# Kernel optimization log

Hardware: AMD Instinct MI355X
Metric: run time of the kernel (lower is better)

## Reference

```python
import jax, jax.numpy as jnp
import numpy as np

B, N, C, H, L, M, V, NC = 8, 2048, 512, 8, 8, 128, 32000, 2
HD = C // H          # head dim = 64
HID = 4 * C          # MLP hidden = 2048
SCALE = HD ** -0.5
LN_EPS = 1e-5
FEAT_EPS = 1e-6


def _orth_matrix(d, m, rng):
    # gaussian_orthogonal_random_matrix: stack QR blocks of d x d
    blocks = []
    n_full, m_rem = divmod(m, d)
    for _ in range(n_full):
        Q, _ = np.linalg.qr(rng.standard_normal((d, d)))
        blocks.append(Q)
    if m_rem > 0:
        Q, _ = np.linalg.qr(rng.standard_normal((d, d)))
        blocks.append(Q[:, :m_rem])
    return np.concatenate(blocks, axis=1)


def setup_inputs() -> dict:
    key = jax.random.key(0)
    ks = jax.random.split(key, 32)
    rng = np.random.default_rng(0)

    def w(i, shape, s=0.02):
        return jax.random.normal(ks[i], shape, jnp.float32) * s

    proj = jnp.asarray(
        np.stack([np.stack([_orth_matrix(HD, M, rng) for _ in range(H)]) for _ in range(L)]),
        jnp.float32)  # [L, H, HD, M]

    inp = {
        "input_ids": jax.random.randint(ks[0], (B, N), 0, V),
        "attention_mask": jnp.ones((B, N), jnp.int32),
        "tok_emb": w(1, (V, C)),
        "cls": w(2, (1, 1, C)),
        "pos": w(3, (N + 1, C)),
        "ln1_g": jnp.ones((L, C), jnp.float32),
        "ln1_b": jnp.zeros((L, C), jnp.float32),
        "qW": w(4, (L, C, C)), "qb": jnp.zeros((L, C), jnp.float32),
        "kW": w(5, (L, C, C)), "kb": jnp.zeros((L, C), jnp.float32),
        "vW": w(6, (L, C, C)), "vb": jnp.zeros((L, C), jnp.float32),
        "oW": w(7, (L, C, C)), "ob": jnp.zeros((L, C), jnp.float32),
        "proj": proj,
        "ln2_g": jnp.ones((L, C), jnp.float32),
        "ln2_b": jnp.zeros((L, C), jnp.float32),
        "fc1W": w(8, (L, C, HID)), "fc1b": jnp.zeros((L, HID), jnp.float32),
        "fc2W": w(9, (L, HID, C)), "fc2b": jnp.zeros((L, C), jnp.float32),
        "lnf_g": jnp.ones((C,), jnp.float32),
        "lnf_b": jnp.zeros((C,), jnp.float32),
        "headW": w(10, (C, NC)),
        "headb": jnp.zeros((NC,), jnp.float32),
    }
    return inp


def _ln(x, g, b):
    mu = jnp.mean(x, axis=-1, keepdims=True)
    var = jnp.mean((x - mu) ** 2, axis=-1, keepdims=True)
    return (x - mu) * jax.lax.rsqrt(var + LN_EPS) * g + b


def _softmax_feature(x, p):
    # x: [B,Nt,H,HD], p: [H,HD,M]
    xw = jnp.einsum('bnhd,hdm->bnhm', x, p)
    x_sq = 0.5 * jnp.sum(x * x, axis=-1, keepdims=True)
    mx = jnp.max(xw, axis=-1, keepdims=True)
    return jnp.exp(xw - mx) * jnp.exp(mx - x_sq) + FEAT_EPS


def reference(input_ids, attention_mask, tok_emb, cls, pos, ln1_g, ln1_b,
              qW, qb, kW, kb, vW, vb, oW, ob, proj, ln2_g, ln2_b,
              fc1W, fc1b, fc2W, fc2b, lnf_g, lnf_b, headW, headb):
    x = tok_emb[input_ids]                                   # [B,N,C]
    x = jnp.concatenate([jnp.broadcast_to(cls, (B, 1, C)), x], axis=1)  # [B,Nt,C]
    x = x + pos[None]
    mask = jnp.concatenate(
        [jnp.ones((B, 1), x.dtype), attention_mask.astype(x.dtype)], axis=1)  # [B,Nt]
    mfeat = mask[:, :, None, None]

    Nt = N + 1
    for i in range(L):
        # Performer attention (FAVOR+)
        y = _ln(x, ln1_g[i], ln1_b[i])
        q = (y @ qW[i] + qb[i]).reshape(B, Nt, H, HD) * SCALE
        k = (y @ kW[i] + kb[i]).reshape(B, Nt, H, HD) * mfeat
        v = (y @ vW[i] + vb[i]).reshape(B, Nt, H, HD) * mfeat
        qf = _softmax_feature(q, proj[i])                    # [B,Nt,H,M]
        kf = _softmax_feature(k, proj[i])
        kv = jnp.einsum('bnhm,bnhd->bhmd', kf, v)            # [B,H,M,HD]
        ksum = jnp.sum(kf, axis=1)                           # [B,H,M]
        denom = jnp.maximum(jnp.einsum('bnhm,bhm->bhn', qf, ksum), 1e-6)[..., None]
        ctx = jnp.einsum('bnhm,bhmd->bhnd', qf, kv) / denom  # [B,H,Nt,HD]
        out = ctx.transpose(0, 2, 1, 3).reshape(B, Nt, C)
        x = x + (out @ oW[i] + ob[i])
        # MLP (exact GELU, as nn.GELU default)
        y = _ln(x, ln2_g[i], ln2_b[i])
        h = jax.nn.gelu(y @ fc1W[i] + fc1b[i], approximate=False)
        x = x + (h @ fc2W[i] + fc2b[i])

    x = _ln(x, lnf_g, lnf_b)
    return x[:, 0] @ headW + headb                           # [B,NC]
```

## Files before the change

kernel.cpp:

```cpp
#include <hip/hip_runtime.h>
#include <cmath>
#include <cstdint>
#include <cstddef>

#define B_ 8
#define N_ 2048
#define NT 2049
#define NP 2080
#define C_ 512
#define H_ 8
#define HD_ 64
#define L_ 8
#define M_ 128
#define HID_ 2048
#define NC_ 2
#define BNT (B_*NT)
#define RP (B_*NP)
#define SCALE_ 0.125f
#define LN_EPS_ 1e-5f
#define FEAT_EPS_ 1e-6f

#define MODE_GELU  2
#define MODE_RESID 3

typedef unsigned short u16;
typedef unsigned short u16x8 __attribute__((ext_vector_type(8)));
typedef short frag __attribute__((ext_vector_type(8)));
typedef float f32x4 __attribute__((ext_vector_type(4)));

constexpr size_t F_X    = 0;
constexpr size_t F_KVP  = F_X   + (size_t)RP*512;
constexpr size_t F_KSP  = F_KVP + (size_t)4*64*8192;
constexpr size_t F_KV   = F_KSP + (size_t)4*64*128;
constexpr size_t F_KS   = F_KV  + (size_t)64*M_*HD_;
constexpr size_t F_QKVB = F_KS  + (size_t)64*M_;
constexpr size_t F_END  = F_QKVB + 1536;
constexpr size_t S_BASE = 2 * F_END;
constexpr size_t S_Y    = S_BASE;
constexpr size_t S_V    = S_Y  + (size_t)RP*512;
constexpr size_t S_KF   = S_V  + (size_t)RP*512;
constexpr size_t S_QF   = S_KF + (size_t)RP*1024;
constexpr size_t S_WQKV = S_QF + (size_t)RP*1024;
constexpr size_t S_WO   = S_WQKV + (size_t)1536*512;
constexpr size_t S_WF1  = S_WO   + (size_t)512*512;
constexpr size_t S_WF2  = S_WF1  + (size_t)2048*512;
constexpr size_t S_PT   = S_WF2  + (size_t)512*2048;
constexpr size_t S_END  = S_PT   + (size_t)8*128*64;
constexpr size_t WS_BYTES = S_END * 2;

__device__ __forceinline__ float wave_reduce(float v) {
#pragma unroll
  for (int off = 32; off > 0; off >>= 1) v += __shfl_down(v, off, 64);
  return v;
}
__device__ __forceinline__ float b2f(u16 u) {
  union { float f; uint32_t i; } v; v.i = ((uint32_t)u) << 16; return v.f;
}
__device__ __forceinline__ u16 f2b(float f) {
  union { float f; uint32_t i; } v; v.f = f;
  uint32_t r = v.i + 0x7FFF + ((v.i >> 16) & 1);
  return (u16)(r >> 16);
}
__device__ __forceinline__ void gstage(const u16* g, u16* lds_base, int lane) {
#if __has_builtin(__builtin_amdgcn_global_load_lds)
  __builtin_amdgcn_global_load_lds((const __attribute__((address_space(1))) void*)g,
      (__attribute__((address_space(3))) void*)lds_base, 16, 0, 0);
#else
  *(u16x8*)(lds_base + lane * 8) = *(const u16x8*)g;
#endif
}
__device__ __forceinline__ void xcd_swz(int& bx, int& by) {
  int gx = gridDim.x;
  int nwg = gx * gridDim.y;
  int hw = blockIdx.x + blockIdx.y * gx;
  if (nwg & 7) { bx = blockIdx.x; by = blockIdx.y; return; }
  int cpx = nwg >> 3;
  int swz = (hw & 7) * cpx + (hw >> 3);
  bx = swz % gx; by = swz / gx;
}

__global__ __launch_bounds__(256) void embed_k(const int* __restrict__ ids,
    const float* __restrict__ tok, const float* __restrict__ cls,
    const float* __restrict__ pos, float* __restrict__ X) {
  int row = blockIdx.x;
  int b = row / NT, n = row - b * NT;
  int t = threadIdx.x;
  const float* src = (n == 0) ? cls : tok + (size_t)ids[b * N_ + n - 1] * C_;
  size_t rp = (size_t)b * NP + n;
  X[rp * C_ + t]       = src[t]       + pos[(size_t)n * C_ + t];
  X[rp * C_ + t + 256] = src[t + 256] + pos[(size_t)n * C_ + t + 256];
}

__global__ __launch_bounds__(256) void wconv_k(
    const float* __restrict__ qW, const float* __restrict__ kW,
    const float* __restrict__ vW, const float* __restrict__ oW,
    const float* __restrict__ f1W, const float* __restrict__ f2W,
    const float* __restrict__ projL,
    const float* __restrict__ qb, const float* __restrict__ kb,
    const float* __restrict__ vb,
    u16* __restrict__ Wqkv, u16* __restrict__ Wo,
    u16* __restrict__ Wf1, u16* __restrict__ Wf2,
    u16* __restrict__ PT, float* __restrict__ QKVB) {
  __shared__ float tile[32][33];
  int bid = blockIdx.x, t = threadIdx.x;
  if (bid >= 3104) {
    int i = (bid - 3104) * 256 + t;
    QKVB[i] = (i < 512) ? qb[i] : (i < 1024) ? kb[i - 512] : vb[i - 1024];
    return;
  }
  if (bid >= 3072) {
    int base = (bid - 3072) * 2048 + t * 8;
#pragma unroll
    for (int j = 0; j < 8; ++j) {
      int idx = base + j;
      int h = idx >> 13, rem = idx & 8191, m = rem >> 6, d = rem & 63;
      PT[idx] = f2b(projL[(size_t)h * 8192 + d * 128 + m]);
    }
    return;
  }
  int ti = t >> 5, tj = t & 31;
  const float* src; u16* dst; int k0, n0, ldn, ldk, scol;
  if (bid < 768) {
    int tk = bid & 15, tn = bid >> 4;
    k0 = tk * 32; n0 = tn * 32;
    int sel = n0 >> 9; scol = n0 & 511;
    src = (sel == 0) ? qW : (sel == 1) ? kW : vW;
    ldn = 512; dst = Wqkv; ldk = 512;
  } else if (bid < 1024) {
    int b2 = bid - 768;
    int tk = b2 & 15, tn = b2 >> 4;
    k0 = tk * 32; n0 = tn * 32; scol = n0;
    src = oW; ldn = 512; dst = Wo; ldk = 512;
  } else if (bid < 2048) {
    int b2 = bid - 1024;
    int tk = b2 & 15, tn = b2 >> 4;
    k0 = tk * 32; n0 = tn * 32; scol = n0;
    src = f1W; ldn = 2048; dst = Wf1; ldk = 512;
  } else {
    int b2 = bid - 2048;
    int tk = b2 & 63, tn = b2 >> 6;
    k0 = tk * 32; n0 = tn * 32; scol = n0;
    src = f2W; ldn = 512; dst = Wf2; ldk = 2048;
  }
  const float* sp = src + (size_t)k0 * ldn + scol;
  u16* dp = dst + (size_t)n0 * ldk + k0;
#pragma unroll
  for (int p = 0; p < 4; ++p)
    tile[ti + p * 8][tj] = sp[(size_t)(ti + p * 8) * ldn + tj];
  __syncthreads();
#pragma unroll
  for (int p = 0; p < 4; ++p)
    dp[(size_t)(ti + p * 8) * ldk + tj] = f2b(tile[tj][ti + p * 8]);
}

__global__ __launch_bounds__(256) void ln_bf_k(const float* __restrict__ X,
    const float* __restrict__ g, const float* __restrict__ b,
    u16* __restrict__ Y) {
  int w = threadIdx.x >> 6, lane = threadIdx.x & 63;
  int row = blockIdx.x * 4 + w;
  const float* xr = X + (size_t)row * C_;
  float v[8];
  *(float4*)&v[0] = *(const float4*)(xr + lane * 8);
  *(float4*)&v[4] = *(const float4*)(xr + lane * 8 + 4);
  float s = 0.f;
#pragma unroll
  for (int j = 0; j < 8; ++j) s += v[j];
  s = wave_reduce(s);
  float mu = __shfl(s, 0, 64) * (1.0f / C_);
  float sq = 0.f;
#pragma unroll
  for (int j = 0; j < 8; ++j) { float d = v[j] - mu; sq = fmaf(d, d, sq); }
  sq = wave_reduce(sq);
  float rs = rsqrtf(__shfl(sq, 0, 64) * (1.0f / C_) + LN_EPS_);
  float gv[8], bv[8];
  *(float4*)&gv[0] = *(const float4*)(g + lane * 8);
  *(float4*)&gv[4] = *(const float4*)(g + lane * 8 + 4);
  *(float4*)&bv[0] = *(const float4*)(b + lane * 8);
  *(float4*)&bv[4] = *(const float4*)(b + lane * 8 + 4);
  u16x8 o;
#pragma unroll
  for (int j = 0; j < 8; ++j) o[j] = f2b((v[j] - mu) * rs * gv[j] + bv[j]);
  *(u16x8*)(Y + (size_t)row * C_ + lane * 8) = o;
}

__global__ __launch_bounds__(256) void gemm_bf_k(
    const u16* __restrict__ A, int lda,
    const u16* __restrict__ Wt,
    const float* __restrict__ bias,
    float* __restrict__ outF, u16* __restrict__ outB,
    int ldc, int Kdim, int mode) {
  __shared__ __align__(16) u16 As[2][128 * 64];
  __shared__ __align__(16) u16 Bs[2][128 * 64];
  const int t = threadIdx.x, w = t >> 6, l = t & 63;
  int bx, by; xcd_swz(bx, by);
  const int row0 = by * 128, col0 = bx * 128;
  const int wm = w & 1, wn = w >> 1;
  const int lm = l & 15, lkb = l >> 4;
  const int lr = l >> 3, lc = l & 7;
  const int kch = (lc ^ lr) * 8;
  const u16* Ag = A  + (size_t)(row0 + lr) * lda  + kch;
  const u16* Bg = Wt + (size_t)(col0 + lr) * Kdim + kch;
  const int sx = lm & 7;
  f32x4 acc[4][4] = {};
  const int nk = Kdim >> 6;
#pragma unroll
  for (int j = 0; j < 4; ++j) {
    int c8 = w * 4 + j;
    gstage(Ag + (size_t)c8 * 8 * lda , &As[0][c8 * 512], l);
    gstage(Bg + (size_t)c8 * 8 * Kdim, &Bs[0][c8 * 512], l);
  }
  for (int kt = 0; kt < nk; ++kt) {
    const int cur = kt & 1;
    if (kt + 1 < nk) {
      const int k0 = (kt + 1) << 6;
#pragma unroll
      for (int j = 0; j < 4; ++j) {
        int c8 = w * 4 + j;
        gstage(Ag + (size_t)c8 * 8 * lda  + k0, &As[cur ^ 1][c8 * 512], l);
        gstage(Bg + (size_t)c8 * 8 * Kdim + k0, &Bs[cur ^ 1][c8 * 512], l);
      }
      asm volatile("s_waitcnt vmcnt(8)" ::: "memory");
    } else {
      asm volatile("s_waitcnt vmcnt(0)" ::: "memory");
    }
    __builtin_amdgcn_s_barrier();
    __builtin_amdgcn_sched_barrier(0);
#pragma unroll
    for (int ks = 0; ks < 2; ++ks) {
      frag af[4], bf4[4];
#pragma unroll
      for (int i = 0; i < 4; ++i)
        af[i] = *(const frag*)&As[cur][(wm * 64 + i * 16 + lm) * 64 + (((ks * 4 + lkb) ^ sx) * 8)];
#pragma unroll
      for (int j = 0; j < 4; ++j)
        bf4[j] = *(const frag*)&Bs[cur][(wn * 64 + j * 16 + lm) * 64 + (((ks * 4 + lkb) ^ sx) * 8)];
#pragma unroll
      for (int i = 0; i < 4; ++i)
#pragma unroll
        for (int j = 0; j < 4; ++j)
          acc[i][j] = __builtin_amdgcn_mfma_f32_16x16x32_bf16(af[i], bf4[j], acc[i][j], 0, 0, 0);
    }
    __builtin_amdgcn_sched_barrier(0);
    __builtin_amdgcn_s_barrier();
  }
#pragma unroll
  for (int i = 0; i < 4; ++i) {
#pragma unroll
    for (int r = 0; r < 4; ++r) {
      int grow = row0 + wm * 64 + i * 16 + lkb * 4 + r;
      if (mode == MODE_RESID) {
        float* orow = outF + (size_t)grow * ldc + col0;
#pragma unroll
        for (int j = 0; j < 4; ++j) {
          int gc = wn * 64 + j * 16 + lm;
          orow[gc] += acc[i][j][r] + bias[col0 + gc];
        }
      } else {
        u16* orow = outB + (size_t)grow * ldc + col0;
#pragma unroll
        for (int j = 0; j < 4; ++j) {
          int gc = wn * 64 + j * 16 + lm;
          float v = acc[i][j][r] + bias[col0 + gc];
          float u = v * (1.5957691216f + 0.0713548162f * v * v);
          v = v / (1.f + __expf(-u));
          orow[gc] = f2b(v);
        }
      }
    }
  }
}

__global__ __launch_bounds__(256) void gemm_bf64_k(
    const u16* __restrict__ A, int lda,
    const u16* __restrict__ Wt,
    const float* __restrict__ bias,
    float* __restrict__ outF, u16* __restrict__ outB,
    int ldc, int Kdim, int mode) {
  __shared__ __align__(16) u16 As[2][64 * 64];
  __shared__ __align__(16) u16 Bs[2][128 * 64];
  const int t = threadIdx.x, w = t >> 6, l = t & 63;
  int bx, by; xcd_swz(bx, by);
  const int row0 = by * 64, col0 = bx * 128;
  const int wm = w & 1, wn = w >> 1;
  const int lm = l & 15, lkb = l >> 4;
  const int lr = l >> 3, lc = l & 7;
  const int kch = (lc ^ lr) * 8;
  const u16* Ag = A  + (size_t)(row0 + lr) * lda  + kch;
  const u16* Bg = Wt + (size_t)(col0 + lr) * Kdim + kch;
  const int sx = lm & 7;
  f32x4 acc[2][4] = {};
  const int nk = Kdim >> 6;
#pragma unroll
  for (int q = 0; q < 2; ++q) {
    int c8 = w * 2 + q;
    gstage(Ag + (size_t)c8 * 8 * lda, &As[0][c8 * 512], l);
  }
#pragma unroll
  for (int q = 0; q < 4; ++q) {
    int c8 = w * 4 + q;
    gstage(Bg + (size_t)c8 * 8 * Kdim, &Bs[0][c8 * 512], l);
  }
  for (int kt = 0; kt < nk; ++kt) {
    const int cur = kt & 1;
    if (kt + 1 < nk) {
      const int k0 = (kt + 1) << 6;
#pragma unroll
      for (int q = 0; q < 2; ++q) {
        int c8 = w * 2 + q;
        gstage(Ag + (size_t)c8 * 8 * lda + k0, &As[cur ^ 1][c8 * 512], l);
      }
#pragma unroll
      for (int q = 0; q < 4; ++q) {
        int c8 = w * 4 + q;
        gstage(Bg + (size_t)c8 * 8 * Kdim + k0, &Bs[cur ^ 1][c8 * 512], l);
      }
      asm volatile("s_waitcnt vmcnt(6)" ::: "memory");
    } else {
      asm volatile("s_waitcnt vmcnt(0)" ::: "memory");
    }
    __builtin_amdgcn_s_barrier();
    __builtin_amdgcn_sched_barrier(0);
#pragma unroll
    for (int ks = 0; ks < 2; ++ks) {
      frag af[2], bf4[4];
#pragma unroll
      for (int i = 0; i < 2; ++i)
        af[i] = *(const frag*)&As[cur][(wm * 32 + i * 16 + lm) * 64 + (((ks * 4 + lkb) ^ sx) * 8)];
#pragma unroll
      for (int j = 0; j < 4; ++j)
        bf4[j] = *(const frag*)&Bs[cur][(wn * 64 + j * 16 + lm) * 64 + (((ks * 4 + lkb) ^ sx) * 8)];
#pragma unroll
      for (int i = 0; i < 2; ++i)
#pragma unroll
        for (int j = 0; j < 4; ++j)
          acc[i][j] = __builtin_amdgcn_mfma_f32_16x16x32_bf16(af[i], bf4[j], acc[i][j], 0, 0, 0);
    }
    __builtin_amdgcn_sched_barrier(0);
    __builtin_amdgcn_s_barrier();
  }
#pragma unroll
  for (int i = 0; i < 2; ++i) {
#pragma unroll
    for (int r = 0; r < 4; ++r) {
      int grow = row0 + wm * 32 + i * 16 + lkb * 4 + r;
      if (mode == MODE_RESID) {
        float* orow = outF + (size_t)grow * ldc + col0;
#pragma unroll
        for (int j = 0; j < 4; ++j) {
          int gc = wn * 64 + j * 16 + lm;
          orow[gc] += acc[i][j][r] + bias[col0 + gc];
        }
      } else {
        u16* orow = outB + (size_t)grow * ldc + col0;
#pragma unroll
        for (int j = 0; j < 4; ++j) {
          int gc = wn * 64 + j * 16 + lm;
          float v = acc[i][j][r] + bias[col0 + gc];
          float u = v * (1.5957691216f + 0.0713548162f * v * v);
          v = v / (1.f + __expf(-u));
          orow[gc] = f2b(v);
        }
      }
    }
  }
}

__global__ __launch_bounds__(256) void gemmqkv_k(
    const u16* __restrict__ A,
    const u16* __restrict__ Wt,
    const float* __restrict__ bias,
    u16* __restrict__ Vout,
    u16* __restrict__ QF, u16* __restrict__ KF,
    const u16* __restrict__ PT,
    const int* __restrict__ attn) {
  __shared__ __align__(16) u16 As[128 * 64];
  __shared__ __align__(16) u16 Bs[128 * 64];
  __shared__ __align__(16) u16 ptb[128 * 64];
  __shared__ float sxe[128][2];
  const int t = threadIdx.x, w = t >> 6, l = t & 63;
  int bx, by; xcd_swz(bx, by);
  const int cx = bx;
  const int row0 = by * 128, col0 = cx * 128;
  const int wm = w & 1, wn = w >> 1;
  const int lm = l & 15, lkb = l >> 4;
  const int lr = l >> 3, lc = l & 7;
  const int kch = (lc ^ lr) * 8;
  const u16* Ag = A  + (size_t)(row0 + lr) * 512 + kch;
  const u16* Bg = Wt + (size_t)(col0 + lr) * 512 + kch;
  const int sx = lm & 7;
  f32x4 acc[4][4] = {};
  for (int k0 = 0; k0 < 512; k0 += 64) {
    __syncthreads();
#pragma unroll
    for (int j = 0; j < 4; ++j) {
      int c8 = w * 4 + j;
      gstage(Ag + (size_t)c8 * 8 * 512 + k0, &As[c8 * 512], l);
      gstage(Bg + (size_t)c8 * 8 * 512 + k0, &Bs[c8 * 512], l);
    }
    __syncthreads();
#pragma unroll
    for (int ks = 0; ks < 2; ++ks) {
      frag af[4], bf4[4];
#pragma unroll
      for (int i = 0; i < 4; ++i)
        af[i] = *(const frag*)&As[(wm * 64 + i * 16 + lm) * 64 + (((ks * 4 + lkb) ^ sx) * 8)];
#pragma unroll
      for (int j = 0; j < 4; ++j)
        bf4[j] = *(const frag*)&Bs[(wn * 64 + j * 16 + lm) * 64 + (((ks * 4 + lkb) ^ sx) * 8)];
#pragma unroll
      for (int i = 0; i < 4; ++i)
#pragma unroll
        for (int j = 0; j < 4; ++j)
          acc[i][j] = __builtin_amdgcn_mfma_f32_16x16x32_bf16(af[i], bf4[j], acc[i][j], 0, 0, 0);
    }
  }
  if (cx >= 8) {
    int c0v = col0 - 1024;
#pragma unroll
    for (int i = 0; i < 4; ++i) {
#pragma unroll
      for (int r = 0; r < 4; ++r) {
        int grow = row0 + wm * 64 + i * 16 + lkb * 4 + r;
        int bb = grow / NP, nn = grow - bb * NP;
        float mrow = (nn == 0) ? 1.f : ((nn < NT) ? (float)attn[bb * N_ + nn - 1] : 0.f);
        u16* orow = Vout + (size_t)grow * 512 + c0v;
#pragma unroll
        for (int j = 0; j < 4; ++j) {
          int gc = wn * 64 + j * 16 + lm;
          orow[gc] = f2b((acc[i][j][r] + bias[col0 + gc]) * mrow);
        }
      }
    }
    return;
  }
  const bool isq = (cx < 4);
  const int hbase = (isq ? cx : cx - 4) * 2;
  __syncthreads();
  {
    u16* qt = wn ? Bs : As;
#pragma unroll
    for (int i = 0; i < 4; ++i) {
#pragma unroll
      for (int r = 0; r < 4; ++r) {
        int rl = wm * 64 + i * 16 + lkb * 4 + r;
        float mrow;
        if (isq) mrow = SCALE_;
        else {
          int grow = row0 + rl;
          int bb = grow / NP, nn = grow - bb * NP;
          mrow = (nn == 0) ? 1.f : ((nn < NT) ? (float)attn[bb * N_ + nn - 1] : 0.f);
        }
#pragma unroll
        for (int j = 0; j < 4; ++j) {
          int gcc = j * 16 + lm;
          float v = (acc[i][j][r] + bias[col0 + wn * 64 + gcc]) * mrow;
          qt[rl * 64 + (((gcc >> 3) ^ (rl & 7)) * 8) + (gcc & 7)] = f2b(v);
        }
      }
    }
  }
  {
    const u16* Pg = PT + (size_t)hbase * 8192 + (size_t)lr * 64 + kch;
#pragma unroll
    for (int q = 0; q < 4; ++q) {
      int c8 = w * 4 + q;
      gstage(Pg + (size_t)c8 * 8 * 64, &ptb[c8 * 512], l);
    }
  }
  __syncthreads();
  {
    int rowi = t >> 1, hf = t & 1;
    const u16* qq = hf ? Bs : As;
    float s = 0.f;
#pragma unroll
    for (int c = 0; c < 8; ++c) {
      const u16* p = &qq[rowi * 64 + ((c ^ (rowi & 7)) * 8)];
#pragma unroll
      for (int e = 0; e < 8; ++e) { float a = b2f(p[e]); s = fmaf(a, a, s); }
    }
    sxe[rowi][hf] = 0.5f * s;
  }
  __syncthreads();
  u16* OF = isq ? QF : KF;
#pragma unroll
  for (int hp = 0; hp < 2; ++hp) {
    if (hp == 1) {
      __syncthreads();
      const u16* Pg = PT + (size_t)(hbase + 1) * 8192 + (size_t)lr * 64 + kch;
#pragma unroll
      for (int q = 0; q < 4; ++q) {
        int c8 = w * 4 + q;
        gstage(Pg + (size_t)c8 * 8 * 64, &ptb[c8 * 512], l);
      }
      __syncthreads();
    }
    const u16* qt = hp ? Bs : As;
    f32x4 a2[2][8] = {};
#pragma unroll
    for (int ks = 0; ks < 2; ++ks) {
      frag af2[2], bf2[8];
#pragma unroll
      for (int i = 0; i < 2; ++i)
        af2[i] = *(const frag*)&qt[(w * 32 + i * 16 + lm) * 64 + (((ks * 4 + lkb) ^ sx) * 8)];
#pragma unroll
      for (int j = 0; j < 8; ++j)
        bf2[j] = *(const frag*)&ptb[(j * 16 + lm) * 64 + (((ks * 4 + lkb) ^ sx) * 8)];
#pragma unroll
      for (int i = 0; i < 2; ++i)
#pragma unroll
        for (int j = 0; j < 8; ++j)
          a2[i][j] = __builtin_amdgcn_mfma_f32_16x16x32_bf16(af2[i], bf2[j], a2[i][j], 0, 0, 0);
    }
    int hg = hbase + hp;
#pragma unroll
    for (int i = 0; i < 2; ++i) {
#pragma unroll
      for (int r = 0; r < 4; ++r) {
        int R = w * 32 + i * 16 + lkb * 4 + r;
        int grow = row0 + R;
        int bb = grow / NP, nn = grow - bb * NP;
        bool valid = nn < NT;
        float xs = sxe[R][hp];
        u16* orow = OF + (size_t)grow * 1024 + (size_t)hg * 128;
#pragma unroll
        for (int j = 0; j < 8; ++j) {
          int m = j * 16 + lm;
          float v = valid ? (__expf(a2[i][j][r] - xs) + FEAT_EPS_) : 0.f;
          orow[m] = f2b(v);
        }
      }
    }
  }
}

__global__ __launch_bounds__(256) void kvpart_k(const u16* __restrict__ KF,
    const u16* __restrict__ Vb, float* __restrict__ KVP,
    float* __restrict__ KSP) {
  int ci = blockIdx.x, bh = blockIdx.y;
  int b = bh >> 3, h = bh & 7;
  size_t rb0 = (size_t)b * NP + ci * 520;
  __shared__ __align__(16) float kfs[8 * 132];
  __shared__ __align__(16) float vsm[8 * 68];
  int t = threadIdx.x;
  const int d0 = (t & 7) * 8, m0 = (t >> 3) * 4;
  const bool hk = t < 128;
  const bool hv = (t >= 128) && (t < 192);
  const int ktok = t >> 4, kmj = (t & 15) * 8;
  const int vtok = (t - 128) >> 3, vdj = (t & 7) * 8;
  float acc[4][8] = {};
  float ks[4] = {};
  u16x8 rk, rv;
  if (hk) rk = *(const u16x8*)&KF[(rb0 + ktok) * 1024 + h * 128 + kmj];
  if (hv) rv = *(const u16x8*)&Vb[(rb0 + vtok) * 512 + h * 64 + vdj];
  for (int tile = 0; tile < 65; ++tile) {
    if (hk) {
#pragma unroll
      for (int e = 0; e < 8; ++e) kfs[ktok * 132 + kmj + e] = b2f(rk[e]);
    }
    if (hv) {
#pragma unroll
      for (int e = 0; e < 8; ++e) vsm[vtok * 68 + vdj + e] = b2f(rv[e]);
    }
    __syncthreads();
    if (tile + 1 < 65) {
      size_t rb = rb0 + (size_t)(tile + 1) * 8;
      if (hk) rk = *(const u16x8*)&KF[(rb + ktok) * 1024 + h * 128 + kmj];
      if (hv) rv = *(const u16x8*)&Vb[(rb + vtok) * 512 + h * 64 + vdj];
    }
#pragma unroll
    for (int tok = 0; tok < 8; ++tok) {
      float kq[4], va[8];
      *(float4*)&kq[0] = *(const float4*)&kfs[tok * 132 + m0];
      *(float4*)&va[0] = *(const float4*)&vsm[tok * 68 + d0];
      *(float4*)&va[4] = *(const float4*)&vsm[tok * 68 + d0 + 4];
#pragma unroll
      for (int mi = 0; mi < 4; ++mi)
#pragma unroll
        for (int di = 0; di < 8; ++di)
          acc[mi][di] = fmaf(kq[mi], va[di], acc[mi][di]);
      if ((t & 7) == 0) { ks[0] += kq[0]; ks[1] += kq[1]; ks[2] += kq[2]; ks[3] += kq[3]; }
    }
    __syncthreads();
  }
  size_t base = ((size_t)ci * 64 + bh) * 8192;
#pragma unroll
  for (int mi = 0; mi < 4; ++mi)
#pragma unroll
    for (int di = 0; di < 8; ++di)
      KVP[base + (size_t)(m0 + mi) * 64 + d0 + di] = acc[mi][di];
  if ((t & 7) == 0) {
#pragma unroll
    for (int mi = 0; mi < 4; ++mi)
      KSP[((size_t)ci * 64 + bh) * 128 + m0 + mi] = ks[mi];
  }
}

__global__ __launch_bounds__(256) void kvred_k(const float* __restrict__ KVP,
    const float* __restrict__ KSP, float* __restrict__ KV,
    float* __restrict__ KSUM) {
  int bh = blockIdx.x, t = threadIdx.x;
#pragma unroll
  for (int p = 0; p < 32; ++p) {
    int e = p * 256 + t;
    float s = 0.f;
#pragma unroll
    for (int ci = 0; ci < 4; ++ci) s += KVP[((size_t)ci * 64 + bh) * 8192 + e];
    KV[(size_t)bh * 8192 + e] = s;
  }
  if (t < 128) {
    float s = 0.f;
#pragma unroll
    for (int ci = 0; ci < 4; ++ci) s += KSP[((size_t)ci * 64 + bh) * 128 + t];
    KSUM[(size_t)bh * 128 + t] = s;
  }
}

__global__ __launch_bounds__(256) void ctx_k(const u16* __restrict__ QF,
    const float* __restrict__ KVg, const float* __restrict__ KSUM,
    u16* __restrict__ CTXo) {
  __shared__ float qfs[128 * 36];
  __shared__ float kvs[128 * 68];
  __shared__ float ksums[128];
  __shared__ float dls[32];
  __shared__ float dpart[8 * 32];
  int t = threadIdx.x;
  int bx, by; xcd_swz(bx, by);
  int bh = by; int b = bh >> 3, h = bh & 7;
  int n0 = bx * 32;
  size_t rbase = (size_t)b * NP + n0;
#pragma unroll
  for (int p = 0; p < 16; ++p) {
    int e = p * 256 + t; int m = e & 127; int tok = e >> 7;
    qfs[m * 36 + tok] = b2f(QF[(rbase + tok) * 1024 + h * 128 + m]);
  }
#pragma unroll
  for (int p = 0; p < 32; ++p) {
    int e = p * 256 + t;
    kvs[(e >> 6) * 68 + (e & 63)] = KVg[(size_t)bh * 8192 + e];
  }
  if (t < 128) ksums[t] = KSUM[bh * 128 + t];
  __syncthreads();
  {
    int j = t & 31, pp = t >> 5;
    float s = 0.f;
#pragma unroll
    for (int mi = 0; mi < 16; ++mi) {
      int m = pp * 16 + mi;
      s = fmaf(qfs[m * 36 + j], ksums[m], s);
    }
    dpart[pp * 32 + j] = s;
  }
  __syncthreads();
  if (t < 32) {
    float den = 0.f;
#pragma unroll
    for (int pp = 0; pp < 8; ++pp) den += dpart[pp * 32 + t];
    dls[t] = 1.f / fmaxf(den, 1e-6f);
  }
  __syncthreads();
  {
    const int d0 = (t & 15) * 4, tok0 = (t >> 4) * 2;
    float acc[2][4] = {};
#pragma unroll 16
    for (int m = 0; m < 128; ++m) {
      float q0 = qfs[m * 36 + tok0];
      float q1 = qfs[m * 36 + tok0 + 1];
      float4 kv4 = *(const float4*)&kvs[m * 68 + d0];
      acc[0][0] = fmaf(q0, kv4.x, acc[0][0]); acc[0][1] = fmaf(q0, kv4.y, acc[0][1]);
      acc[0][2] = fmaf(q0, kv4.z, acc[0][2]); acc[0][3] = fmaf(q0, kv4.w, acc[0][3]);
      acc[1][0] = fmaf(q1, kv4.x, acc[1][0]); acc[1][1] = fmaf(q1, kv4.y, acc[1][1]);
      acc[1][2] = fmaf(q1, kv4.z, acc[1][2]); acc[1][3] = fmaf(q1, kv4.w, acc[1][3]);
    }
#pragma unroll
    for (int r = 0; r < 2; ++r) {
      int n = n0 + tok0 + r;
      if (n >= NT) continue;
      float rd = dls[tok0 + r];
      u16* o = CTXo + (rbase + tok0 + r) * C_ + h * HD_ + d0;
#pragma unroll
      for (int c = 0; c < 4; ++c) o[c] = f2b(acc[r][c] * rd);
    }
  }
}

__global__ __launch_bounds__(256) void final_k(const float* __restrict__ X,
    const float* __restrict__ g, const float* __restrict__ beta,
    const float* __restrict__ hW, const float* __restrict__ hb,
    float* __restrict__ out) {
  int b = blockIdx.x, t = threadIdx.x;
  const float* xr = X + (size_t)b * NP * C_;
  float v0 = xr[t], v1 = xr[t + 256];
  __shared__ float red[4][4];
  float s = wave_reduce(v0 + v1);
  if ((t & 63) == 0) red[0][t >> 6] = s;
  __syncthreads();
  float mu = (red[0][0] + red[0][1] + red[0][2] + red[0][3]) * (1.0f / C_);
  float d0 = v0 - mu, d1 = v1 - mu;
  float s2 = wave_reduce(d0 * d0 + d1 * d1);
  if ((t & 63) == 0) red[1][t >> 6] = s2;
  __syncthreads();
  float var = (red[1][0] + red[1][1] + red[1][2] + red[1][3]) * (1.0f / C_);
  float rs = rsqrtf(var + LN_EPS_);
  float n0 = d0 * rs * g[t] + beta[t];
  float n1 = d1 * rs * g[t + 256] + beta[t + 256];
  float p0 = n0 * hW[t * NC_]     + n1 * hW[(t + 256) * NC_];
  float p1 = n0 * hW[t * NC_ + 1] + n1 * hW[(t + 256) * NC_ + 1];
  float t0 = wave_reduce(p0);
  float t1 = wave_reduce(p1);
  if ((t & 63) == 0) { red[2][t >> 6] = t0; red[3][t >> 6] = t1; }
  __syncthreads();
  if (t == 0) {
    out[b * NC_]     = red[2][0] + red[2][1] + red[2][2] + red[2][3] + hb[0];
    out[b * NC_ + 1] = red[3][0] + red[3][1] + red[3][2] + red[3][3] + hb[1];
  }
}

extern "C" void kernel_launch(void* const* d_in, const int* in_sizes, int n_in,
                              void* d_out, int out_size, void* d_ws, size_t ws_size,
                              hipStream_t stream) {
  if (ws_size < WS_BYTES) return;
  const int*   ids   = (const int*)d_in[0];
  const int*   attn  = (const int*)d_in[1];
  const float* tok   = (const float*)d_in[2];
  const float* cls   = (const float*)d_in[3];
  const float* pos   = (const float*)d_in[4];
  const float* ln1g  = (const float*)d_in[5];
  const float* ln1b  = (const float*)d_in[6];
  const float* qW    = (const float*)d_in[7];
  const float* qb    = (const float*)d_in[8];
  const float* kW    = (const float*)d_in[9];
  const float* kb    = (const float*)d_in[10];
  const float* vW    = (const float*)d_in[11];
  const float* vb    = (const float*)d_in[12];
  const float* oW    = (const float*)d_in[13];
  const float* ob    = (const float*)d_in[14];
  const float* proj  = (const float*)d_in[15];
  const float* ln2g  = (const float*)d_in[16];
  const float* ln2b  = (const float*)d_in[17];
  const float* fc1W  = (const float*)d_in[18];
  const float* fc1b  = (const float*)d_in[19];
  const float* fc2W  = (const float*)d_in[20];
  const float* fc2b  = (const float*)d_in[21];
  const float* lnfg  = (const float*)d_in[22];
  const float* lnfb  = (const float*)d_in[23];
  const float* headW = (const float*)d_in[24];
  const float* headb = (const float*)d_in[25];

  float* ws  = (float*)d_ws;
  u16*   wsu = (u16*)d_ws;
  float* X    = ws + F_X;
  float* KVP  = ws + F_KVP;
  float* KSP  = ws + F_KSP;
  float* KV   = ws + F_KV;
  float* KSUM = ws + F_KS;
  float* QKVB = ws + F_QKVB;
  u16* Ybf  = wsu + S_Y;
  u16* CTXb = wsu + S_Y;
  u16* Vb   = wsu + S_V;
  u16* HB   = wsu + S_V;
  u16* KFb  = wsu + S_KF;
  u16* QFb  = wsu + S_QF;
  u16* Wqkv = wsu + S_WQKV;
  u16* Wo   = wsu + S_WO;
  u16* Wf1  = wsu + S_WF1;
  u16* Wf2  = wsu + S_WF2;
  u16* PT   = wsu + S_PT;

  embed_k<<<BNT, 256, 0, stream>>>(ids, tok, cls, pos, X);
  for (int i = 0; i < L_; ++i) {
    wconv_k<<<3110, 256, 0, stream>>>(qW + (size_t)i * C_ * C_, kW + (size_t)i * C_ * C_,
        vW + (size_t)i * C_ * C_, oW + (size_t)i * C_ * C_,
        fc1W + (size_t)i * C_ * HID_, fc2W + (size_t)i * HID_ * C_,
        proj + (size_t)i * H_ * HD_ * M_,
        qb + i * C_, kb + i * C_, vb + i * C_,
        Wqkv, Wo, Wf1, Wf2, PT, QKVB);
    ln_bf_k<<<RP / 4, 256, 0, stream>>>(X, ln1g + i * C_, ln1b + i * C_, Ybf);
    gemmqkv_k<<<dim3(12, 130), 256, 0, stream>>>(Ybf, Wqkv, QKVB,
        Vb, QFb, KFb, PT, attn);
    kvpart_k<<<dim3(4, 64), 256, 0, stream>>>(KFb, Vb, KVP, KSP);
    kvred_k<<<64, 256, 0, stream>>>(KVP, KSP, KV, KSUM);
    ctx_k<<<dim3(65, 64), 256, 0, stream>>>(QFb, KV, KSUM, CTXb);
    gemm_bf64_k<<<dim3(4, 260), 256, 0, stream>>>(CTXb, 512, Wo, ob + i * C_,
        X, nullptr, 512, 512, MODE_RESID);
    ln_bf_k<<<RP / 4, 256, 0, stream>>>(X, ln2g + i * C_, ln2b + i * C_, Ybf);
    gemm_bf_k<<<dim3(16, 130), 256, 0, stream>>>(Ybf, 512, Wf1,
        fc1b + i * HID_, nullptr, HB, 2048, 512, MODE_GELU);
    gemm_bf64_k<<<dim3(4, 260), 256, 0, stream>>>(HB, 2048, Wf2,
        fc2b + i * C_, X, nullptr, 512, 2048, MODE_RESID);
  }
  final_k<<<B_, 256, 0, stream>>>(X, lnfg, lnfb, headW, headb, (float*)d_out);
}
```

Before: 3.117 ms.

## Use 256x256 tile 8-wave GEMM with interleaved staging for fc1

Replaces the 128x128 four-wave fc1 GEMM with a 256x256 tile, eight-wave kernel. Each wave computes 128x64 and the A/B halves are loaded in four phases interleaved with MFMA blocks, using s_setprio around the MFMAs. This raises arithmetic intensity per loaded byte and overlaps global-to-LDS staging with compute. It doubles LDS usage to 128KB per block, and the grid drops to 520 blocks, which may hurt occupancy and tail balance. The partial vmcnt waits and barriers must be exactly right for the phased buffer reuse.

After: 3.425 ms. +9.9%, slower.

```diff
diff --git a/kernel.cpp b/kernel.cpp
--- a/kernel.cpp
+++ b/kernel.cpp
@@ -183,84 +183,133 @@
   *(u16x8*)(Y + (size_t)row * C_ + lane * 8) = o;
 }
 
-__global__ __launch_bounds__(256) void gemm_bf_k(
+__global__ __launch_bounds__(512, 2) void gemm256_k(
     const u16* __restrict__ A, int lda,
     const u16* __restrict__ Wt,
     const float* __restrict__ bias,
     float* __restrict__ outF, u16* __restrict__ outB,
     int ldc, int Kdim, int mode) {
-  __shared__ __align__(16) u16 As[2][128 * 64];
-  __shared__ __align__(16) u16 Bs[2][128 * 64];
+  __shared__ __align__(16) u16 As[2][2][128 * 64];
+  __shared__ __align__(16) u16 Bs[2][2][128 * 64];
   const int t = threadIdx.x, w = t >> 6, l = t & 63;
   int bx, by; xcd_swz(bx, by);
-  const int row0 = by * 128, col0 = bx * 128;
-  const int wm = w & 1, wn = w >> 1;
+  const int row0 = by * 256, col0 = bx * 256;
+  const int wm = w >> 2, wn = w & 3;
   const int lm = l & 15, lkb = l >> 4;
   const int lr = l >> 3, lc = l & 7;
   const int kch = (lc ^ lr) * 8;
+  const int sx = lm & 7;
+  const int bcl = (wn & 1) * 64;
   const u16* Ag = A  + (size_t)(row0 + lr) * lda  + kch;
   const u16* Bg = Wt + (size_t)(col0 + lr) * Kdim + kch;
-  const int sx = lm & 7;
-  f32x4 acc[4][4] = {};
+  f32x4 acc[8][4] = {};
   const int nk = Kdim >> 6;
-#pragma unroll
-  for (int j = 0; j < 4; ++j) {
-    int c8 = w * 4 + j;
-    gstage(Ag + (size_t)c8 * 8 * lda , &As[0][c8 * 512], l);
-    gstage(Bg + (size_t)c8 * 8 * Kdim, &Bs[0][c8 * 512], l);
-  }
+
+#define STAGE_A(kt_, h_, b_) do {                                            \
+    _Pragma("unroll")                                                        \
+    for (int q = 0; q < 2; ++q) {                                            \
+      int rg = w * 2 + q;                                                    \
+      gstage(Ag + (size_t)((h_) * 128 + rg * 8) * lda + (kt_) * 64,          \
+             &As[b_][h_][rg * 512], l);                                      \
+    } } while (0)
+#define STAGE_B(kt_, h_, b_) do {                                            \
+    _Pragma("unroll")                                                        \
+    for (int q = 0; q < 2; ++q) {                                            \
+      int rg = w * 2 + q;                                                    \
+      gstage(Bg + (size_t)((h_) * 128 + rg * 8) * Kdim + (kt_) * 64,         \
+             &Bs[b_][h_][rg * 512], l);                                      \
+    } } while (0)
+#define RD_A(Ah_, rh_, ks_, dst_) do {                                       \
+    _Pragma("unroll")                                                        \
+    for (int i_ = 0; i_ < 4; ++i_)                                           \
+      dst_[i_] = *(const frag*)&(Ah_)[((rh_) * 64 + i_ * 16 + lm) * 64 +     \
+                                      ((((ks_) * 4 + lkb) ^ sx) * 8)];       \
+    } while (0)
+#define RD_B(Bh_, ks_, dst_) do {                                            \
+    _Pragma("unroll")                                                        \
+    for (int j_ = 0; j_ < 4; ++j_)                                           \
+      dst_[j_] = *(const frag*)&(Bh_)[(bcl + j_ * 16 + lm) * 64 +            \
+                                      ((((ks_) * 4 + lkb) ^ sx) * 8)];       \
+    } while (0)
+#define MFMA16(rbase_, af_, bf_) do {                                        \
+    _Pragma("unroll")                                                        \
+    for (int i_ = 0; i_ < 4; ++i_)                                           \
+      _Pragma("unroll")                                                      \
+      for (int j_ = 0; j_ < 4; ++j_)                                         \
+        acc[(rbase_) + i_][j_] = __builtin_amdgcn_mfma_f32_16x16x32_bf16(    \
+            af_[i_], bf_[j_], acc[(rbase_) + i_][j_], 0, 0, 0);              \
+    } while (0)
+
+  STAGE_A(0, 0, 0); STAGE_A(0, 1, 0); STAGE_B(0, 0, 0); STAGE_B(0, 1, 0);
+
   for (int kt = 0; kt < nk; ++kt) {
-    const int cur = kt & 1;
-    if (kt + 1 < nk) {
-      const int k0 = (kt + 1) << 6;
-#pragma unroll
-      for (int j = 0; j < 4; ++j) {
-        int c8 = w * 4 + j;
-        gstage(Ag + (size_t)c8 * 8 * lda  + k0, &As[cur ^ 1][c8 * 512], l);
-        gstage(Bg + (size_t)c8 * 8 * Kdim + k0, &Bs[cur ^ 1][c8 * 512], l);
-      }
-      asm volatile("s_waitcnt vmcnt(8)" ::: "memory");
+    const int pb = kt & 1;
+    const bool more = (kt + 1 < nk);
+    const u16* Ah = &As[pb][wm][0];
+    const u16* Bh = &Bs[pb][wn >> 1][0];
+    frag af0[4], af1[4], bf0[4], bf1[4];
+    if (more) {
+      STAGE_A(kt + 1, 0, pb ^ 1);
+      asm volatile("s_waitcnt vmcnt(2)" ::: "memory");
     } else {
       asm volatile("s_waitcnt vmcnt(0)" ::: "memory");
     }
     __builtin_amdgcn_s_barrier();
     __builtin_amdgcn_sched_barrier(0);
-#pragma unroll
-    for (int ks = 0; ks < 2; ++ks) {
-      frag af[4], bf4[4];
-#pragma unroll
-      for (int i = 0; i < 4; ++i)
-        af[i] = *(const frag*)&As[cur][(wm * 64 + i * 16 + lm) * 64 + (((ks * 4 + lkb) ^ sx) * 8)];
-#pragma unroll
-      for (int j = 0; j < 4; ++j)
-        bf4[j] = *(const frag*)&Bs[cur][(wn * 64 + j * 16 + lm) * 64 + (((ks * 4 + lkb) ^ sx) * 8)];
-#pragma unroll
-      for (int i = 0; i < 4; ++i)
-#pragma unroll
-        for (int j = 0; j < 4; ++j)
-          acc[i][j] = __builtin_amdgcn_mfma_f32_16x16x32_bf16(af[i], bf4[j], acc[i][j], 0, 0, 0);
-    }
+    RD_A(Ah, 0, 0, af0);
+    RD_B(Bh, 0, bf0);
+    __builtin_amdgcn_s_setprio(1);
+    MFMA16(0, af0, bf0);
+    __builtin_amdgcn_s_setprio(0);
     __builtin_amdgcn_sched_barrier(0);
     __builtin_amdgcn_s_barrier();
-  }
-#pragma unroll
-  for (int i = 0; i < 4; ++i) {
+    if (more) STAGE_A(kt + 1, 1, pb ^ 1);
+    RD_A(Ah, 1, 0, af1);
+    __builtin_amdgcn_s_setprio(1);
+    MFMA16(4, af1, bf0);
+    __builtin_amdgcn_s_setprio(0);
+    __builtin_amdgcn_sched_barrier(0);
+    __builtin_amdgcn_s_barrier();
+    if (more) STAGE_B(kt + 1, 0, pb ^ 1);
+    RD_A(Ah, 0, 1, af0);
+    RD_B(Bh, 1, bf1);
+    __builtin_amdgcn_s_setprio(1);
+    MFMA16(0, af0, bf1);
+    __builtin_amdgcn_s_setprio(0);
+    __builtin_amdgcn_sched_barrier(0);
+    __builtin_amdgcn_s_barrier();
+    if (more) STAGE_B(kt + 1, 1, pb ^ 1);
+    RD_A(Ah, 1, 1, af1);
+    __builtin_amdgcn_s_setprio(1);
+    MFMA16(4, af1, bf1);
+    __builtin_amdgcn_s_setprio(0);
+    __builtin_amdgcn_sched_barrier(0);
+    __builtin_amdgcn_s_barrier();
+  }
+#undef STAGE_A
+#undef STAGE_B
+#undef RD_A
+#undef RD_B
+#undef MFMA16
+
+#pragma unroll
+  for (int rf = 0; rf < 8; ++rf) {
 #pragma unroll
     for (int r = 0; r < 4; ++r) {
-      int grow = row0 + wm * 64 + i * 16 + lkb * 4 + r;
+      int grow = row0 + wm * 128 + rf * 16 + lkb * 4 + r;
       if (mode == MODE_RESID) {
         float* orow = outF + (size_t)grow * ldc + col0;
 #pragma unroll
-        for (int j = 0; j < 4; ++j) {
-          int gc = wn * 64 + j * 16 + lm;
-          orow[gc] += acc[i][j][r] + bias[col0 + gc];
+        for (int cf = 0; cf < 4; ++cf) {
+          int gc = wn * 64 + cf * 16 + lm;
+          orow[gc] += acc[rf][cf][r] + bias[col0 + gc];
         }
       } else {
         u16* orow = outB + (size_t)grow * ldc + col0;
 #pragma unroll
-        for (int j = 0; j < 4; ++j) {
-          int gc = wn * 64 + j * 16 + lm;
-          float v = acc[i][j][r] + bias[col0 + gc];
+        for (int cf = 0; cf < 4; ++cf) {
+          int gc = wn * 64 + cf * 16 + lm;
+          float v = acc[rf][cf][r] + bias[col0 + gc];
           float u = v * (1.5957691216f + 0.0713548162f * v * v);
           v = v / (1.f + __expf(-u));
           orow[gc] = f2b(v);
@@ -783,7 +832,7 @@
     gemm_bf64_k<<<dim3(4, 260), 256, 0, stream>>>(CTXb, 512, Wo, ob + i * C_,
         X, nullptr, 512, 512, MODE_RESID);
     ln_bf_k<<<RP / 4, 256, 0, stream>>>(X, ln2g + i * C_, ln2b + i * C_, Ybf);
-    gemm_bf_k<<<dim3(16, 130), 256, 0, stream>>>(Ybf, 512, Wf1,
+    gemm256_k<<<dim3(8, 65), 512, 0, stream>>>(Ybf, 512, Wf1,
         fc1b + i * HID_, nullptr, HB, 2048, 512, MODE_GELU);
     gemm_bf64_k<<<dim3(4, 260), 256, 0, stream>>>(HB, 2048, Wf2,
         fc2b + i * C_, X, nullptr, 512, 2048, MODE_RESID);
```

## Split KV reduction into eight chunks and transpose ctx query feature layout

Applied to the files above, without the earlier changes.

The kv partial-sum kernel now launches eight sequence chunks per batch-head instead of four, so more workgroups run in parallel and each does a shorter serial loop. The extra partials go into a second scratch area that aliases the Y/CTX buffer, and the reduce kernel sums both areas. ctx_k stores query features token-major so each thread can read them with float4 loads. Padding rows are now zeroed explicitly in embed and the QKV/ctx epilogues so garbage in pad rows cannot turn into NaN. The cost is more partial-sum traffic and a reliance on the aliased buffer being free while kvpart and kvred run.

After: 3.362 ms. +7.9%, slower.

```diff
diff --git a/kernel.cpp b/kernel.cpp
--- a/kernel.cpp
+++ b/kernel.cpp
@@ -83,10 +83,15 @@
     const float* __restrict__ tok, const float* __restrict__ cls,
     const float* __restrict__ pos, float* __restrict__ X) {
   int row = blockIdx.x;
-  int b = row / NT, n = row - b * NT;
+  int b = row / NP, n = row - b * NP;
   int t = threadIdx.x;
+  size_t rp = (size_t)row;
+  if (n >= NT) {
+    X[rp * C_ + t]       = 0.f;
+    X[rp * C_ + t + 256] = 0.f;
+    return;
+  }
   const float* src = (n == 0) ? cls : tok + (size_t)ids[b * N_ + n - 1] * C_;
-  size_t rp = (size_t)b * NP + n;
   X[rp * C_ + t]       = src[t]       + pos[(size_t)n * C_ + t];
   X[rp * C_ + t + 256] = src[t + 256] + pos[(size_t)n * C_ + t + 256];
 }
@@ -427,7 +432,8 @@
 #pragma unroll
         for (int j = 0; j < 4; ++j) {
           int gc = wn * 64 + j * 16 + lm;
-          orow[gc] = f2b((acc[i][j][r] + bias[col0 + gc]) * mrow);
+          float vv = acc[i][j][r] + bias[col0 + gc];
+          orow[gc] = f2b(mrow == 0.f ? 0.f : vv * mrow);
         }
       }
     }
@@ -453,7 +459,8 @@
 #pragma unroll
         for (int j = 0; j < 4; ++j) {
           int gcc = j * 16 + lm;
-          float v = (acc[i][j][r] + bias[col0 + wn * 64 + gcc]) * mrow;
+          float v = acc[i][j][r] + bias[col0 + wn * 64 + gcc];
+          v = (mrow == 0.f) ? 0.f : v * mrow;
           qt[rl * 64 + (((gcc >> 3) ^ (rl & 7)) * 8) + (gcc & 7)] = f2b(v);
         }
       }
@@ -535,10 +542,13 @@
 
 __global__ __launch_bounds__(256) void kvpart_k(const u16* __restrict__ KF,
     const u16* __restrict__ Vb, float* __restrict__ KVP,
-    float* __restrict__ KSP) {
+    float* __restrict__ KVP2, float* __restrict__ KSP,
+    float* __restrict__ KSP2) {
   int ci = blockIdx.x, bh = blockIdx.y;
   int b = bh >> 3, h = bh & 7;
-  size_t rb0 = (size_t)b * NP + ci * 520;
+  const int start = (ci < 4) ? ci * 264 : 1056 + (ci - 4) * 256;
+  const int ntile = (ci < 4) ? 33 : 32;
+  size_t rb0 = (size_t)b * NP + start;
   __shared__ __align__(16) float kfs[8 * 132];
   __shared__ __align__(16) float vsm[8 * 68];
   int t = threadIdx.x;
@@ -552,7 +562,7 @@
   u16x8 rk, rv;
   if (hk) rk = *(const u16x8*)&KF[(rb0 + ktok) * 1024 + h * 128 + kmj];
   if (hv) rv = *(const u16x8*)&Vb[(rb0 + vtok) * 512 + h * 64 + vdj];
-  for (int tile = 0; tile < 65; ++tile) {
+  for (int tile = 0; tile < ntile; ++tile) {
     if (hk) {
 #pragma unroll
       for (int e = 0; e < 8; ++e) kfs[ktok * 132 + kmj + e] = b2f(rk[e]);
@@ -562,7 +572,7 @@
       for (int e = 0; e < 8; ++e) vsm[vtok * 68 + vdj + e] = b2f(rv[e]);
     }
     __syncthreads();
-    if (tile + 1 < 65) {
+    if (tile + 1 < ntile) {
       size_t rb = rb0 + (size_t)(tile + 1) * 8;
       if (hk) rk = *(const u16x8*)&KF[(rb + ktok) * 1024 + h * 128 + kmj];
       if (hv) rv = *(const u16x8*)&Vb[(rb + vtok) * 512 + h * 64 + vdj];
@@ -582,21 +592,25 @@
     }
     __syncthreads();
   }
-  size_t base = ((size_t)ci * 64 + bh) * 8192;
+  float* dk  = (ci < 4) ? KVP : KVP2;
+  float* dsp = (ci < 4) ? KSP : KSP2;
+  const int cs = ci & 3;
+  size_t base = ((size_t)cs * 64 + bh) * 8192;
 #pragma unroll
   for (int mi = 0; mi < 4; ++mi)
 #pragma unroll
     for (int di = 0; di < 8; ++di)
-      KVP[base + (size_t)(m0 + mi) * 64 + d0 + di] = acc[mi][di];
+      dk[base + (size_t)(m0 + mi) * 64 + d0 + di] = acc[mi][di];
   if ((t & 7) == 0) {
 #pragma unroll
     for (int mi = 0; mi < 4; ++mi)
-      KSP[((size_t)ci * 64 + bh) * 128 + m0 + mi] = ks[mi];
+      dsp[((size_t)cs * 64 + bh) * 128 + m0 + mi] = ks[mi];
   }
 }
 
 __global__ __launch_bounds__(256) void kvred_k(const float* __restrict__ KVP,
-    const float* __restrict__ KSP, float* __restrict__ KV,
+    const float* __restrict__ KVP2, const float* __restrict__ KSP,
+    const float* __restrict__ KSP2, float* __restrict__ KV,
     float* __restrict__ KSUM) {
   int bh = blockIdx.x, t = threadIdx.x;
 #pragma unroll
@@ -604,13 +618,19 @@
     int e = p * 256 + t;
     float s = 0.f;
 #pragma unroll
-    for (int ci = 0; ci < 4; ++ci) s += KVP[((size_t)ci * 64 + bh) * 8192 + e];
+    for (int ci = 0; ci < 4; ++ci) {
+      s += KVP [((size_t)ci * 64 + bh) * 8192 + e];
+      s += KVP2[((size_t)ci * 64 + bh) * 8192 + e];
+    }
     KV[(size_t)bh * 8192 + e] = s;
   }
   if (t < 128) {
     float s = 0.f;
 #pragma unroll
-    for (int ci = 0; ci < 4; ++ci) s += KSP[((size_t)ci * 64 + bh) * 128 + t];
+    for (int ci = 0; ci < 4; ++ci) {
+      s += KSP [((size_t)ci * 64 + bh) * 128 + t];
+      s += KSP2[((size_t)ci * 64 + bh) * 128 + t];
+    }
     KSUM[(size_t)bh * 128 + t] = s;
   }
 }
@@ -618,7 +638,7 @@
 __global__ __launch_bounds__(256) void ctx_k(const u16* __restrict__ QF,
     const float* __restrict__ KVg, const float* __restrict__ KSUM,
     u16* __restrict__ CTXo) {
-  __shared__ float qfs[128 * 36];
+  __shared__ float qfs[32 * 132];
   __shared__ float kvs[128 * 68];
   __shared__ float ksums[128];
   __shared__ float dls[32];
@@ -631,7 +651,7 @@
 #pragma unroll
   for (int p = 0; p < 16; ++p) {
     int e = p * 256 + t; int m = e & 127; int tok = e >> 7;
-    qfs[m * 36 + tok] = b2f(QF[(rbase + tok) * 1024 + h * 128 + m]);
+    qfs[tok * 132 + m] = b2f(QF[(rbase + tok) * 1024 + h * 128 + m]);
   }
 #pragma unroll
   for (int p = 0; p < 32; ++p) {
@@ -646,7 +666,7 @@
 #pragma unroll
     for (int mi = 0; mi < 16; ++mi) {
       int m = pp * 16 + mi;
-      s = fmaf(qfs[m * 36 + j], ksums[m], s);
+      s = fmaf(qfs[j * 132 + m], ksums[m], s);
     }
     dpart[pp * 32 + j] = s;
   }
@@ -661,24 +681,31 @@
   {
     const int d0 = (t & 15) * 4, tok0 = (t >> 4) * 2;
     float acc[2][4] = {};
-#pragma unroll 16
-    for (int m = 0; m < 128; ++m) {
-      float q0 = qfs[m * 36 + tok0];
-      float q1 = qfs[m * 36 + tok0 + 1];
-      float4 kv4 = *(const float4*)&kvs[m * 68 + d0];
-      acc[0][0] = fmaf(q0, kv4.x, acc[0][0]); acc[0][1] = fmaf(q0, kv4.y, acc[0][1]);
-      acc[0][2] = fmaf(q0, kv4.z, acc[0][2]); acc[0][3] = fmaf(q0, kv4.w, acc[0][3]);
-      acc[1][0] = fmaf(q1, kv4.x, acc[1][0]); acc[1][1] = fmaf(q1, kv4.y, acc[1][1]);
-      acc[1][2] = fmaf(q1, kv4.z, acc[1][2]); acc[1][3] = fmaf(q1, kv4.w, acc[1][3]);
+    const float* q0r = &qfs[tok0 * 132];
+    const float* q1r = &qfs[(tok0 + 1) * 132];
+#pragma unroll 8
+    for (int m4 = 0; m4 < 128; m4 += 4) {
+      float4 q0v = *(const float4*)&q0r[m4];
+      float4 q1v = *(const float4*)&q1r[m4];
+#pragma unroll
+      for (int i = 0; i < 4; ++i) {
+        float4 kv4 = *(const float4*)&kvs[(m4 + i) * 68 + d0];
+        float q0 = (i == 0) ? q0v.x : (i == 1) ? q0v.y : (i == 2) ? q0v.z : q0v.w;
+        float q1 = (i == 0) ? q1v.x : (i == 1) ? q1v.y : (i == 2) ? q1v.z : q1v.w;
+        acc[0][0] = fmaf(q0, kv4.x, acc[0][0]); acc[0][1] = fmaf(q0, kv4.y, acc[0][1]);
+        acc[0][2] = fmaf(q0, kv4.z, acc[0][2]); acc[0][3] = fmaf(q0, kv4.w, acc[0][3]);
+        acc[1][0] = fmaf(q1, kv4.x, acc[1][0]); acc[1][1] = fmaf(q1, kv4.y, acc[1][1]);
+        acc[1][2] = fmaf(q1, kv4.z, acc[1][2]); acc[1][3] = fmaf(q1, kv4.w, acc[1][3]);
+      }
     }
 #pragma unroll
     for (int r = 0; r < 2; ++r) {
       int n = n0 + tok0 + r;
-      if (n >= NT) continue;
-      float rd = dls[tok0 + r];
+      bool pad = (n >= NT);
+      float rd = pad ? 0.f : dls[tok0 + r];
       u16* o = CTXo + (rbase + tok0 + r) * C_ + h * HD_ + d0;
 #pragma unroll
-      for (int c = 0; c < 4; ++c) o[c] = f2b(acc[r][c] * rd);
+      for (int c = 0; c < 4; ++c) o[c] = f2b(pad ? 0.f : acc[r][c] * rd);
     }
   }
 }
@@ -756,6 +783,8 @@
   float* QKVB = ws + F_QKVB;
   u16* Ybf  = wsu + S_Y;
   u16* CTXb = wsu + S_Y;
+  float* KVP2 = (float*)(wsu + S_Y);
+  float* KSP2 = KVP2 + (size_t)4 * 64 * 8192;
   u16* Vb   = wsu + S_V;
   u16* HB   = wsu + S_V;
   u16* KFb  = wsu + S_KF;
@@ -766,7 +795,7 @@
   u16* Wf2  = wsu + S_WF2;
   u16* PT   = wsu + S_PT;
 
-  embed_k<<<BNT, 256, 0, stream>>>(ids, tok, cls, pos, X);
+  embed_k<<<RP, 256, 0, stream>>>(ids, tok, cls, pos, X);
   for (int i = 0; i < L_; ++i) {
     wconv_k<<<3110, 256, 0, stream>>>(qW + (size_t)i * C_ * C_, kW + (size_t)i * C_ * C_,
         vW + (size_t)i * C_ * C_, oW + (size_t)i * C_ * C_,
@@ -777,8 +806,8 @@
     ln_bf_k<<<RP / 4, 256, 0, stream>>>(X, ln1g + i * C_, ln1b + i * C_, Ybf);
     gemmqkv_k<<<dim3(12, 130), 256, 0, stream>>>(Ybf, Wqkv, QKVB,
         Vb, QFb, KFb, PT, attn);
-    kvpart_k<<<dim3(4, 64), 256, 0, stream>>>(KFb, Vb, KVP, KSP);
-    kvred_k<<<64, 256, 0, stream>>>(KVP, KSP, KV, KSUM);
+    kvpart_k<<<dim3(8, 64), 256, 0, stream>>>(KFb, Vb, KVP, KVP2, KSP, KSP2);
+    kvred_k<<<64, 256, 0, stream>>>(KVP, KVP2, KSP, KSP2, KV, KSUM);
     ctx_k<<<dim3(65, 64), 256, 0, stream>>>(QFb, KV, KSUM, CTXb);
     gemm_bf64_k<<<dim3(4, 260), 256, 0, stream>>>(CTXb, 512, Wo, ob + i * C_,
         X, nullptr, 512, 512, MODE_RESID);
```
